# Optimization experiments

Measured on AMD Instinct MI355X. Metric: run time of the kernel, lower is better.

Reference implementation:

```python
import jax, jax.numpy as jnp
import numpy as np

B, H, L = 4096, 1024, 4


def _lstm_cell(x, h, c, Wih, Whh, bih, bhh):
    # gates: [B, 4H], PyTorch gate order i, f, g, o
    gates = x @ Wih.T + bih + h @ Whh.T + bhh
    i, f, g, o = jnp.split(gates, 4, axis=-1)
    i = jax.nn.sigmoid(i)
    f = jax.nn.sigmoid(f)
    g = jnp.tanh(g)
    o = jax.nn.sigmoid(o)
    c2 = f * c + i * g
    h2 = o * jnp.tanh(c2)
    return h2, c2


def setup_inputs() -> dict:
    key = jax.random.key(0)
    ks = jax.random.split(key, 7)
    scale = 1.0 / np.sqrt(H)  # PyTorch LSTMCell init range
    return {
        "x": jax.random.normal(ks[0], (B, H), jnp.float32),
        "h0": jax.random.normal(ks[1], (B, H, L), jnp.float32),
        "c0": jax.random.normal(ks[2], (B, H, L), jnp.float32),
        "W_ih": jax.random.normal(ks[3], (L, 4 * H, H), jnp.float32) * scale,
        "W_hh": jax.random.normal(ks[4], (L, 4 * H, H), jnp.float32) * scale,
        "b_ih": jax.random.normal(ks[5], (L, 4 * H), jnp.float32) * scale,
        "b_hh": jax.random.normal(ks[6], (L, 4 * H), jnp.float32) * scale,
    }


def reference(x, h0, c0, W_ih, W_hh, b_ih, b_hh):
    # Multi-layer LSTM cell: layer i consumes the hidden output of layer i-1
    # (dropout=None -> identity between layers). prev states indexed on last dim.
    lstm_input = x
    hs, cs = [], []
    for i in range(L):
        h_i, c_i = _lstm_cell(lstm_input, h0[:, :, i], c0[:, :, i],
                              W_ih[i], W_hh[i], b_ih[i], b_hh[i])
        lstm_input = h_i
        hs.append(h_i)
        cs.append(c_i)
    # torch.stack -> [L, B, H]; permute(1, 2, 0) -> [B, H, L]
    next_hidden = jnp.stack(hs, axis=-1)
    next_cell = jnp.stack(cs, axis=-1)
    return next_hidden, next_cell
```

## Files before the change

### kernel.cpp

```cpp
#include <hip/hip_runtime.h>
#include <cstddef>

#define BATCH 4096
#define HID   1024
#define NLAY  4
#define NG    4096
#define KTOT  2048
#define BH    (BATCH * HID)

typedef short short8 __attribute__((ext_vector_type(8)));
typedef float f32x4  __attribute__((ext_vector_type(4)));

__device__ __forceinline__ unsigned short f2bf(float f) {
    union { float f; unsigned u; } v; v.f = f;
    unsigned r = v.u + 0x7fffu + ((v.u >> 16) & 1u);
    return (unsigned short)(r >> 16);
}

__device__ __forceinline__ float sigm_f(float x) {
    return 1.0f / (1.0f + __expf(-x));
}
__device__ __forceinline__ float tanh_f(float x) {
    float e = __expf(-2.0f * fabsf(x));
    float r = (1.0f - e) / (1.0f + e);
    return copysignf(r, x);
}

#define GLOAD_LDS16(g, l)                                                            \
    __builtin_amdgcn_global_load_lds(                                                \
        (const __attribute__((address_space(1))) void*)(g),                          \
        (__attribute__((address_space(3))) void*)(l), 16, 0, 0)

__global__ __launch_bounds__(256) void prep_weights(
    const float* __restrict__ Wih, const float* __restrict__ Whh,
    unsigned short* __restrict__ Wb)
{
    size_t t    = (size_t)blockIdx.x * 256 + threadIdx.x;
    size_t base = t * 4;
    size_t row  = base >> 11;
    int    k    = (int)(base & (KTOT - 1));
    const float* src = (k < HID) ? (Wih + row * HID + k)
                                 : (Whh + row * HID + (k - HID));
    float4 v = *(const float4*)src;
    ushort4 o; o.x = f2bf(v.x); o.y = f2bf(v.y); o.z = f2bf(v.z); o.w = f2bf(v.w);
    *(ushort4*)(Wb + base) = o;
}

__global__ __launch_bounds__(256) void prep_bias(
    const float* __restrict__ bih, const float* __restrict__ bhh,
    float* __restrict__ bias)
{
    int i = blockIdx.x * 256 + threadIdx.x;
    bias[i] = bih[i] + bhh[i];
}

__global__ __launch_bounds__(256) void prep_misc(
    const float* __restrict__ x, const float* __restrict__ h0,
    const float* __restrict__ c0,
    unsigned short* __restrict__ A0, unsigned short* __restrict__ A1,
    unsigned short* __restrict__ A2, unsigned short* __restrict__ A3,
    float* __restrict__ cc)
{
    int idx = blockIdx.x * 256 + threadIdx.x;
    int b = idx >> 10, h = idx & (HID - 1);
    float4 hv = *(const float4*)(h0 + (size_t)idx * NLAY);
    A0[(size_t)b * KTOT + h]       = f2bf(x[idx]);
    A0[(size_t)b * KTOT + HID + h] = f2bf(hv.x);
    A1[(size_t)b * KTOT + HID + h] = f2bf(hv.y);
    A2[(size_t)b * KTOT + HID + h] = f2bf(hv.z);
    A3[(size_t)b * KTOT + HID + h] = f2bf(hv.w);
    if (cc) {
        float4 cv = *(const float4*)(c0 + (size_t)idx * NLAY);
        cc[idx]          = cv.x;
        cc[BH + idx]     = cv.y;
        cc[2 * BH + idx] = cv.z;
        cc[3 * BH + idx] = cv.w;
    }
}

template<bool LM>
__global__ __launch_bounds__(256, 2) void gemm_lstm_fused(
    const unsigned short* __restrict__ A,
    const unsigned short* __restrict__ W,
    const float* __restrict__ bias,
    const float* cin,
    float* cout,
    float* __restrict__ hout,
    unsigned short* __restrict__ Anext,
    int layer)
{
    __shared__ unsigned short ldsA[128 * 64];
    __shared__ unsigned short ldsB[128 * 64];

    const int tid  = threadIdx.x;
    const int wave = tid >> 6;
    const int lane = tid & 63;
    const int bn = blockIdx.x, bm = blockIdx.y;
    const int wm = wave >> 1, wn = wave & 1;

    f32x4 acc[4][4] = {};

    const int srow8 = lane >> 3;
    const int scol  = (((lane & 7) ^ srow8) << 3);
    const unsigned short* Ag = A + (size_t)(bm * 128 + wave * 32 + srow8) * KTOT + scol;
    const unsigned short* Wg[4];
#pragma unroll
    for (int j = 0; j < 4; ++j) {
        int s    = wave * 32 + j * 8 + srow8;
        int wrow = ((s >> 4) & 3) * HID + bn * 32 + (s >> 6) * 16 + (s & 15);
        Wg[j] = W + (size_t)wrow * KTOT + scol;
    }

    const int rrow = lane & 15;
    const int rkey = lane & 7;

    for (int k0 = 0; k0 < KTOT; k0 += 64) {
#pragma unroll
        for (int j = 0; j < 4; ++j) {
            GLOAD_LDS16(Ag + (size_t)(j * 8) * KTOT + k0, &ldsA[(wave * 32 + j * 8) * 64]);
            GLOAD_LDS16(Wg[j] + k0,                        &ldsB[(wave * 32 + j * 8) * 64]);
        }
        __syncthreads();
#pragma unroll
        for (int kk = 0; kk < 2; ++kk) {
            const int ro = ((((lane >> 4) + kk * 4) ^ rkey) << 3);
            short8 af[4], bf[4];
#pragma unroll
            for (int m = 0; m < 4; ++m)
                af[m] = *(const short8*)&ldsA[(wm * 64 + m * 16 + rrow) * 64 + ro];
#pragma unroll
            for (int n = 0; n < 4; ++n)
                bf[n] = *(const short8*)&ldsB[(wn * 64 + n * 16 + rrow) * 64 + ro];
#pragma unroll
            for (int m = 0; m < 4; ++m)
#pragma unroll
                for (int n = 0; n < 4; ++n)
                    acc[m][n] = __builtin_amdgcn_mfma_f32_16x16x32_bf16(
                        af[m], bf[n], acc[m][n], 0, 0, 0);
        }
        __syncthreads();
    }

    const int h = bn * 32 + wn * 16 + (lane & 15);
    float bv[4];
#pragma unroll
    for (int n = 0; n < 4; ++n) bv[n] = bias[n * HID + h];

#pragma unroll
    for (int m = 0; m < 4; ++m) {
        const int b0 = bm * 128 + wm * 64 + m * 16 + ((lane >> 4) << 2);
#pragma unroll
        for (int r = 0; r < 4; ++r) {
            const int b = b0 + r;
            const size_t idx2 = LM ? ((size_t)b * HID + h)
                                   : (((size_t)b * HID + h) * NLAY + layer);
            float iv = sigm_f(acc[m][0][r] + bv[0]);
            float fv = sigm_f(acc[m][1][r] + bv[1]);
            float gv = tanh_f(acc[m][2][r] + bv[2]);
            float ov = sigm_f(acc[m][3][r] + bv[3]);
            float c2 = fv * cin[idx2] + iv * gv;
            float h2 = ov * tanh_f(c2);
            cout[idx2] = c2;
            hout[idx2] = h2;
            if (Anext) Anext[(size_t)b * KTOT + h] = f2bf(h2);
        }
    }
}

__global__ __launch_bounds__(256) void interleave(
    const float* __restrict__ hT, const float* __restrict__ cc,
    float* __restrict__ outH, float* __restrict__ outC)
{
    int idx = blockIdx.x * 256 + threadIdx.x;
    float4 hv = { hT[idx], hT[BH + idx], hT[2 * BH + idx], hT[3 * BH + idx] };
    float4 cv = { cc[idx], cc[BH + idx], cc[2 * BH + idx], cc[3 * BH + idx] };
    *(float4*)(outH + (size_t)idx * NLAY) = hv;
    *(float4*)(outC + (size_t)idx * NLAY) = cv;
}

extern "C" void kernel_launch(void* const* d_in, const int* in_sizes, int n_in,
                              void* d_out, int out_size, void* d_ws, size_t ws_size,
                              hipStream_t stream)
{
    const float* x   = (const float*)d_in[0];
    const float* h0  = (const float*)d_in[1];
    const float* c0  = (const float*)d_in[2];
    const float* Wih = (const float*)d_in[3];
    const float* Whh = (const float*)d_in[4];
    const float* bih = (const float*)d_in[5];
    const float* bhh = (const float*)d_in[6];

    float* outH = (float*)d_out;
    float* outC = outH + (size_t)BH * NLAY;

    char* ws = (char*)d_ws;
    unsigned short* Wb   = (unsigned short*)(ws);
    float*          bias = (float*)(ws + 67108864);
    unsigned short* Ap[4];
    Ap[0] = (unsigned short*)(ws + 67174400);
    Ap[1] = (unsigned short*)(ws + 83951616);
    Ap[2] = (unsigned short*)(ws + 100728832);
    Ap[3] = (unsigned short*)(ws + 117506048);

    const bool lm = (ws_size >= 268500992ULL);
    float* cc = lm ? (float*)(ws + 134283264) : nullptr;
    float* hT = lm ? (float*)(ws + 201392128) : nullptr;

    prep_weights<<<32768, 256, 0, stream>>>(Wih, Whh, Wb);
    prep_bias<<<64, 256, 0, stream>>>(bih, bhh, bias);
    prep_misc<<<BH / 256, 256, 0, stream>>>(x, h0, c0,
                                            Ap[0], Ap[1], Ap[2], Ap[3], cc);

    const dim3 grid(HID / 32, BATCH / 128);
    for (int l = 0; l < NLAY; ++l) {
        unsigned short* An = (l < NLAY - 1) ? Ap[l + 1] : nullptr;
        const unsigned short* Wl = Wb + (size_t)l * NG * KTOT;
        const float* bl = bias + l * NG;
        if (lm) {
            gemm_lstm_fused<true><<<grid, 256, 0, stream>>>(
                Ap[l], Wl, bl, cc + (size_t)l * BH, cc + (size_t)l * BH,
                hT + (size_t)l * BH, An, l);
        } else {
            gemm_lstm_fused<false><<<grid, 256, 0, stream>>>(
                Ap[l], Wl, bl, c0, outC, outH, An, l);
        }
    }

    if (lm) interleave<<<BH / 256, 256, 0, stream>>>(hT, cc, outH, outC);
}
```

Baseline: 683.1 us.

## Rewrite LSTM GEMM as 256x256-tile, 512-thread, double-buffered phased pipeline

Replaces the 128x128-tile single-buffer GEMM with a 256-batch by 64-hidden (256 gate rows) tile on 512 threads, with double-buffered LDS. Global-to-LDS loads for the next K step are interleaved across four MFMA phases, with explicit vmcnt waits, barriers and setprio. The aim is to overlap memory traffic with matrix math and raise data reuse per tile. It also drops the fallback path for small workspaces, so the larger workspace is now always assumed. The LDS footprint grows and occupancy falls to one block per CU.

```diff
diff --git a/kernel.cpp b/kernel.cpp
--- a/kernel.cpp
+++ b/kernel.cpp
@@ -7,6 +7,7 @@
 #define NG    4096
 #define KTOT  2048
 #define BH    (BATCH * HID)
+#define NT    (KTOT / 64)
 
 typedef short short8 __attribute__((ext_vector_type(8)));
 typedef float f32x4  __attribute__((ext_vector_type(4)));
@@ -69,91 +70,152 @@
     A1[(size_t)b * KTOT + HID + h] = f2bf(hv.y);
     A2[(size_t)b * KTOT + HID + h] = f2bf(hv.z);
     A3[(size_t)b * KTOT + HID + h] = f2bf(hv.w);
-    if (cc) {
-        float4 cv = *(const float4*)(c0 + (size_t)idx * NLAY);
-        cc[idx]          = cv.x;
-        cc[BH + idx]     = cv.y;
-        cc[2 * BH + idx] = cv.z;
-        cc[3 * BH + idx] = cv.w;
-    }
-}
-
-template<bool LM>
-__global__ __launch_bounds__(256, 2) void gemm_lstm_fused(
+    float4 cv = *(const float4*)(c0 + (size_t)idx * NLAY);
+    cc[idx]          = cv.x;
+    cc[BH + idx]     = cv.y;
+    cc[2 * BH + idx] = cv.z;
+    cc[3 * BH + idx] = cv.w;
+}
+
+#define FENCE() asm volatile("" ::: "memory")
+#define BARRIER() do { FENCE(); __builtin_amdgcn_s_barrier(); FENCE(); } while (0)
+
+__global__ __launch_bounds__(512, 1) void gemm_lstm_8ph(
     const unsigned short* __restrict__ A,
     const unsigned short* __restrict__ W,
     const float* __restrict__ bias,
     const float* cin,
     float* cout,
     float* __restrict__ hout,
-    unsigned short* __restrict__ Anext,
-    int layer)
-{
-    __shared__ unsigned short ldsA[128 * 64];
-    __shared__ unsigned short ldsB[128 * 64];
+    unsigned short* __restrict__ Anext)
+{
+    __shared__ unsigned short ldsA[2 * 2 * 128 * 64];
+    __shared__ unsigned short ldsB[2 * 2 * 128 * 64];
 
     const int tid  = threadIdx.x;
-    const int wave = tid >> 6;
+    const int wid  = tid >> 6;
     const int lane = tid & 63;
+    const int wm = wid >> 2, wn = wid & 3;
     const int bn = blockIdx.x, bm = blockIdx.y;
-    const int wm = wave >> 1, wn = wave & 1;
-
-    f32x4 acc[4][4] = {};
-
-    const int srow8 = lane >> 3;
-    const int scol  = (((lane & 7) ^ srow8) << 3);
-    const unsigned short* Ag = A + (size_t)(bm * 128 + wave * 32 + srow8) * KTOT + scol;
-    const unsigned short* Wg[4];
-#pragma unroll
-    for (int j = 0; j < 4; ++j) {
-        int s    = wave * 32 + j * 8 + srow8;
-        int wrow = ((s >> 4) & 3) * HID + bn * 32 + (s >> 6) * 16 + (s & 15);
-        Wg[j] = W + (size_t)wrow * KTOT + scol;
-    }
+
+    f32x4 acc[8][4] = {};
+
+    const int srow  = tid >> 3;
+    const int sswz  = ((tid & 7) ^ (srow & 7)) << 3;
+    const int dLds  = srow * 64 + (tid & 7) * 8;
+    const unsigned short* Ag = A + (size_t)(bm * 256 + srow) * KTOT + sswz;
+    const unsigned short* Wg[2][2];
+#pragma unroll
+    for (int half = 0; half < 2; ++half)
+#pragma unroll
+        for (int j = 0; j < 2; ++j) {
+            int s    = half * 128 + j * 64 + srow;
+            int wrow = ((s >> 4) & 3) * HID + bn * 64 + ((s >> 6) & 3) * 16 + (s & 15);
+            Wg[half][j] = W + (size_t)wrow * KTOT + sswz;
+        }
+
+#define STG_A(buf, half, kt) do {                                                     \
+    GLOAD_LDS16(Ag + (size_t)((half) * 128) * KTOT + (size_t)(kt) * 64,               \
+                &ldsA[(buf) * 16384 + (half) * 8192 + dLds]);                         \
+    GLOAD_LDS16(Ag + (size_t)((half) * 128 + 64) * KTOT + (size_t)(kt) * 64,          \
+                &ldsA[(buf) * 16384 + (half) * 8192 + 4096 + dLds]); } while (0)
+#define STG_B(buf, half, kt) do {                                                     \
+    GLOAD_LDS16(Wg[half][0] + (size_t)(kt) * 64,                                      \
+                &ldsB[(buf) * 16384 + (half) * 8192 + dLds]);                         \
+    GLOAD_LDS16(Wg[half][1] + (size_t)(kt) * 64,                                      \
+                &ldsB[(buf) * 16384 + (half) * 8192 + 4096 + dLds]); } while (0)
 
     const int rrow = lane & 15;
     const int rkey = lane & 7;
-
-    for (int k0 = 0; k0 < KTOT; k0 += 64) {
-#pragma unroll
-        for (int j = 0; j < 4; ++j) {
-            GLOAD_LDS16(Ag + (size_t)(j * 8) * KTOT + k0, &ldsA[(wave * 32 + j * 8) * 64]);
-            GLOAD_LDS16(Wg[j] + k0,                        &ldsB[(wave * 32 + j * 8) * 64]);
-        }
-        __syncthreads();
-#pragma unroll
-        for (int kk = 0; kk < 2; ++kk) {
-            const int ro = ((((lane >> 4) + kk * 4) ^ rkey) << 3);
-            short8 af[4], bf[4];
-#pragma unroll
-            for (int m = 0; m < 4; ++m)
-                af[m] = *(const short8*)&ldsA[(wm * 64 + m * 16 + rrow) * 64 + ro];
-#pragma unroll
-            for (int n = 0; n < 4; ++n)
-                bf[n] = *(const short8*)&ldsB[(wn * 64 + n * 16 + rrow) * 64 + ro];
-#pragma unroll
-            for (int m = 0; m < 4; ++m)
-#pragma unroll
-                for (int n = 0; n < 4; ++n)
-                    acc[m][n] = __builtin_amdgcn_mfma_f32_16x16x32_bf16(
-                        af[m], bf[n], acc[m][n], 0, 0, 0);
-        }
-        __syncthreads();
+    const int ro0  = (((lane >> 4) + 0) ^ rkey) << 3;
+    const int ro1  = (((lane >> 4) + 4) ^ rkey) << 3;
+    const int aB   = wm * 8192 + rrow * 64;
+    const int bB   = (wn >> 1) * 8192 + ((wn & 1) * 64 + rrow) * 64;
+
+#define LDA(cb, m, kk) (*(const short8*)&ldsA[(cb) + aB + (m) * 1024 + ((kk) ? ro1 : ro0)])
+#define LDB(cb, n, kk) (*(const short8*)&ldsB[(cb) + bB + (n) * 1024 + ((kk) ? ro1 : ro0)])
+
+#define MFMA_PAIR(m0_)                                                                \
+    do {                                                                              \
+        __builtin_amdgcn_s_setprio(1);                                                \
+        _Pragma("unroll")                                                             \
+        for (int n = 0; n < 4; ++n) {                                                 \
+            acc[m0_][n]     = __builtin_amdgcn_mfma_f32_16x16x32_bf16(                \
+                af[0][0], bf[n][0], acc[m0_][n], 0, 0, 0);                            \
+            acc[m0_][n]     = __builtin_amdgcn_mfma_f32_16x16x32_bf16(                \
+                af[0][1], bf[n][1], acc[m0_][n], 0, 0, 0);                            \
+            acc[m0_ + 1][n] = __builtin_amdgcn_mfma_f32_16x16x32_bf16(                \
+                af[1][0], bf[n][0], acc[m0_ + 1][n], 0, 0, 0);                        \
+            acc[m0_ + 1][n] = __builtin_amdgcn_mfma_f32_16x16x32_bf16(                \
+                af[1][1], bf[n][1], acc[m0_ + 1][n], 0, 0, 0);                        \
+        }                                                                             \
+        __builtin_amdgcn_s_setprio(0);                                                \
+    } while (0)
+
+    STG_A(0, 0, 0); STG_A(0, 1, 0);
+    STG_B(0, 0, 0); STG_B(0, 1, 0);
+    STG_B(1, 0, 1); STG_B(1, 1, 1);
+    asm volatile("s_waitcnt vmcnt(4)" ::: "memory");
+    BARRIER();
+
+    for (int u = 0; u < NT; ++u) {
+        const int cur = u & 1, nxt = cur ^ 1;
+        const int cA = cur * 16384;
+        short8 bf[4][2];
+        {
+            short8 af[2][2];
+#pragma unroll
+            for (int n = 0; n < 4; ++n) { bf[n][0] = LDB(cA, n, 0); bf[n][1] = LDB(cA, n, 1); }
+            af[0][0] = LDA(cA, 0, 0); af[0][1] = LDA(cA, 0, 1);
+            af[1][0] = LDA(cA, 1, 0); af[1][1] = LDA(cA, 1, 1);
+            if (u + 1 < NT) STG_A(nxt, 0, u + 1);
+            BARRIER();
+            MFMA_PAIR(0);
+            BARRIER();
+        }
+        {
+            short8 af[2][2];
+            af[0][0] = LDA(cA, 2, 0); af[0][1] = LDA(cA, 2, 1);
+            af[1][0] = LDA(cA, 3, 0); af[1][1] = LDA(cA, 3, 1);
+            if (u + 1 < NT) STG_A(nxt, 1, u + 1);
+            BARRIER();
+            MFMA_PAIR(2);
+            BARRIER();
+        }
+        {
+            short8 af[2][2];
+            af[0][0] = LDA(cA, 4, 0); af[0][1] = LDA(cA, 4, 1);
+            af[1][0] = LDA(cA, 5, 0); af[1][1] = LDA(cA, 5, 1);
+            if (u + 2 < NT) STG_B(cur, 0, u + 2);
+            BARRIER();
+            MFMA_PAIR(4);
+            BARRIER();
+        }
+        {
+            short8 af[2][2];
+            af[0][0] = LDA(cA, 6, 0); af[0][1] = LDA(cA, 6, 1);
+            af[1][0] = LDA(cA, 7, 0); af[1][1] = LDA(cA, 7, 1);
+            if (u + 2 < NT) STG_B(cur, 1, u + 2);
+            if (u < NT - 2) { asm volatile("s_waitcnt vmcnt(4)" ::: "memory"); }
+            else            { asm volatile("s_waitcnt vmcnt(0)" ::: "memory"); }
+            BARRIER();
+            MFMA_PAIR(6);
+            BARRIER();
+        }
     }
 
-    const int h = bn * 32 + wn * 16 + (lane & 15);
+    const int h = bn * 64 + wn * 16 + (lane & 15);
     float bv[4];
 #pragma unroll
     for (int n = 0; n < 4; ++n) bv[n] = bias[n * HID + h];
 
 #pragma unroll
-    for (int m = 0; m < 4; ++m) {
-        const int b0 = bm * 128 + wm * 64 + m * 16 + ((lane >> 4) << 2);
+    for (int m = 0; m < 8; ++m) {
+        const int b0 = bm * 256 + wm * 128 + m * 16 + ((lane >> 4) << 2);
 #pragma unroll
         for (int r = 0; r < 4; ++r) {
             const int b = b0 + r;
-            const size_t idx2 = LM ? ((size_t)b * HID + h)
-                                   : (((size_t)b * HID + h) * NLAY + layer);
+            const size_t idx2 = (size_t)b * HID + h;
             float iv = sigm_f(acc[m][0][r] + bv[0]);
             float fv = sigm_f(acc[m][1][r] + bv[1]);
             float gv = tanh_f(acc[m][2][r] + bv[2]);
@@ -201,30 +263,21 @@
     Ap[1] = (unsigned short*)(ws + 83951616);
     Ap[2] = (unsigned short*)(ws + 100728832);
     Ap[3] = (unsigned short*)(ws + 117506048);
-
-    const bool lm = (ws_size >= 268500992ULL);
-    float* cc = lm ? (float*)(ws + 134283264) : nullptr;
-    float* hT = lm ? (float*)(ws + 201392128) : nullptr;
+    float* cc = (float*)(ws + 134283264);
+    float* hT = (float*)(ws + 201392128);
 
     prep_weights<<<32768, 256, 0, stream>>>(Wih, Whh, Wb);
     prep_bias<<<64, 256, 0, stream>>>(bih, bhh, bias);
     prep_misc<<<BH / 256, 256, 0, stream>>>(x, h0, c0,
                                             Ap[0], Ap[1], Ap[2], Ap[3], cc);
 
-    const dim3 grid(HID / 32, BATCH / 128);
+    const dim3 grid(HID / 64, BATCH / 256);
     for (int l = 0; l < NLAY; ++l) {
-        unsigned short* An = (l < NLAY - 1) ? Ap[l + 1] : nullptr;
-        const unsigned short* Wl = Wb + (size_t)l * NG * KTOT;
-        const float* bl = bias + l * NG;
-        if (lm) {
-            gemm_lstm_fused<true><<<grid, 256, 0, stream>>>(
-                Ap[l], Wl, bl, cc + (size_t)l * BH, cc + (size_t)l * BH,
-                hT + (size_t)l * BH, An, l);
-        } else {
-            gemm_lstm_fused<false><<<grid, 256, 0, stream>>>(
-                Ap[l], Wl, bl, c0, outC, outH, An, l);
-        }
+        gemm_lstm_8ph<<<grid, 512, 0, stream>>>(
+            Ap[l], Wb + (size_t)l * NG * KTOT, bias + l * NG,
+            cc + (size_t)l * BH, cc + (size_t)l * BH, hT + (size_t)l * BH,
+            (l < NLAY - 1) ? Ap[l + 1] : nullptr);
     }
 
-    if (lm) interleave<<<BH / 256, 256, 0, stream>>>(hT, cc, outH, outC);
-}
+    interleave<<<BH / 256, 256, 0, stream>>>(hT, cc, outH, outC);
+}
```

After: 780.5 us. 14.3% more time.
